# Optimization experiments

Measured on AMD Instinct MI355X. Metric: run time of the kernel, lower is better.

The kernel has to match this reference:

```python
import jax, jax.numpy as jnp
import numpy as np

N_NODES = 100000
N_EDGES = 3200000
BATCH = 16
HIDDEN = 64


def setup_inputs() -> dict:
    key = jax.random.key(0)
    k_mu, k_ei, k_w1, k_b1, k_w2, k_b2 = jax.random.split(key, 6)
    mu = jax.random.normal(k_mu, (BATCH, N_NODES), dtype=jnp.float32)
    edge_index = jax.random.randint(k_ei, (2, N_EDGES), 0, N_NODES, dtype=jnp.int64)
    # MLP params: Linear(1, hidden) -> GELU -> Linear(hidden, 1)
    W1 = jax.random.normal(k_w1, (1, HIDDEN), dtype=jnp.float32) * (1.0 / np.sqrt(1))
    b1 = jax.random.normal(k_b1, (HIDDEN,), dtype=jnp.float32) * 0.02
    W2 = jax.random.normal(k_w2, (HIDDEN, 1), dtype=jnp.float32) * (1.0 / np.sqrt(HIDDEN))
    b2 = jax.random.normal(k_b2, (1,), dtype=jnp.float32) * 0.02
    return {"mu": mu, "edge_index": edge_index, "W1": W1, "b1": b1, "W2": W2, "b2": b2}


def reference(mu, edge_index, W1, b1, W2, b2):
    row, col = edge_index[0], edge_index[1]
    B, N = mu.shape
    # degree of each destination node (clamped at 1)
    deg = jax.ops.segment_sum(jnp.ones_like(row, dtype=mu.dtype), row, num_segments=N)
    deg = jnp.maximum(deg, 1.0)  # [N]
    # batched message aggregation: gather source values, scatter-add to rows
    msgs = mu[:, col].T                                    # [E, B]
    agg = jax.ops.segment_sum(msgs, row, num_segments=N)   # [N, B]
    out = agg.T / deg[None, :]                             # [B, N]
    # tiny MLP applied per scalar: 1 -> hidden -> 1 with exact (erf) GELU
    h = jax.nn.gelu(out[..., None] * W1[0][None, None, :] + b1, approximate=False)  # [B, N, H]
    y = jnp.einsum('bnh,h->bn', h, W2[:, 0]) + b2[0]       # [B, N]
    return y
```

## Files before the change

### kernel.cpp

```cpp
#include <hip/hip_runtime.h>
#include <hip/hip_fp16.h>

#define N_NODES 100000
#define N_EDGES 3200000
#define BATCH   16
#define HIDDEN  64

#define NBINS   512
#define NPB     196
#define CAP_BIN 7168
#define EPB     8192
#define MAXW    14

#define TBLKS   391
#define LBLKS   33

#define LUT_SIZE  8192
#define LUT_LO    (-16.0f)
#define LUT_SCALE (LUT_SIZE / 32.0f)

typedef int v4i __attribute__((ext_vector_type(4)));

__global__ __launch_bounds__(256) void prep_kernel(
    const float* __restrict__ mu, __half* __restrict__ mu_h,
    const float* __restrict__ W1, const float* __restrict__ b1,
    const float* __restrict__ W2, const float* __restrict__ b2,
    float* __restrict__ lut, unsigned int* __restrict__ gcnt) {
  int blk = blockIdx.x;
  int t = threadIdx.x;
  if (blk < TBLKS) {
    int n = blk * 256 + t;
    if (n >= N_NODES) return;
    float4 o[4];
#pragma unroll
    for (int q = 0; q < 4; ++q) {
      o[q].x = mu[(q * 4 + 0) * N_NODES + n];
      o[q].y = mu[(q * 4 + 1) * N_NODES + n];
      o[q].z = mu[(q * 4 + 2) * N_NODES + n];
      o[q].w = mu[(q * 4 + 3) * N_NODES + n];
    }
    __half2 hh[8];
#pragma unroll
    for (int q = 0; q < 4; ++q) {
      hh[2 * q]     = __floats2half2_rn(o[q].x, o[q].y);
      hh[2 * q + 1] = __floats2half2_rn(o[q].z, o[q].w);
    }
    int4 w0 = make_int4(*(int*)&hh[0], *(int*)&hh[1], *(int*)&hh[2], *(int*)&hh[3]);
    int4 w1 = make_int4(*(int*)&hh[4], *(int*)&hh[5], *(int*)&hh[6], *(int*)&hh[7]);
    int4* dst = (int4*)(mu_h + (size_t)n * BATCH);
    dst[0] = w0;
    dst[1] = w1;
  } else if (blk < TBLKS + LBLKS) {
    int i = (blk - TBLKS) * 256 + t;
    if (i > LUT_SIZE) return;
    float x = LUT_LO + (float)i / LUT_SCALE;
    float acc = b2[0];
    for (int h = 0; h < HIDDEN; ++h) {
      float z = fmaf(x, W1[h], b1[h]);
      float g = 0.5f * z * (1.0f + erff(z * 0.70710678118654752f));
      acc = fmaf(g, W2[h], acc);
    }
    lut[i] = acc;
  } else {
    for (int i = t; i < NBINS; i += 256) gcnt[i] = 0u;
  }
}

__global__ __launch_bounds__(512) void partition_kernel(
    const int* __restrict__ ei, unsigned int* __restrict__ gcnt,
    unsigned int* __restrict__ packed) {
  __shared__ int cnt_[NBINS];
  __shared__ int prefix[NBINS];
  __shared__ unsigned int gbase[NBINS];
  __shared__ int wsum[8];
  __shared__ unsigned int stag[EPB];
  __shared__ unsigned short sbin[EPB];

  int t = threadIdx.x;
  int base = blockIdx.x * EPB;
  int nvalid = min(EPB, N_EDGES - base);
  cnt_[t] = 0;
  __syncthreads();

  unsigned int pk[16];
  int bn[16];
  int rk[16];
  if (t * 16 + 16 <= nvalid) {
    const v4i* rp = (const v4i*)(ei + base + t * 16);
    const v4i* cp = (const v4i*)(ei + N_EDGES + base + t * 16);
    v4i rr[4], cc[4];
#pragma unroll
    for (int q = 0; q < 4; ++q) {
      rr[q] = __builtin_nontemporal_load(&rp[q]);
      cc[q] = __builtin_nontemporal_load(&cp[q]);
    }
#pragma unroll
    for (int q = 0; q < 4; ++q) {
#pragma unroll
      for (int u = 0; u < 4; ++u) {
        int k = q * 4 + u;
        int r = rr[q][u];
        int c = cc[q][u];
        int b = r / NPB;
        int rl = r - b * NPB;
        pk[k] = ((unsigned int)rl << 17) | (unsigned int)c;
        bn[k] = b;
      }
    }
#pragma unroll
    for (int k = 0; k < 16; ++k) rk[k] = atomicAdd(&cnt_[bn[k]], 1);
  } else {
#pragma unroll
    for (int k = 0; k < 16; ++k) {
      int e = t * 16 + k;
      if (e < nvalid) {
        int r = ei[base + e];
        int c = ei[N_EDGES + base + e];
        int b = r / NPB;
        int rl = r - b * NPB;
        pk[k] = ((unsigned int)rl << 17) | (unsigned int)c;
        bn[k] = b;
        rk[k] = atomicAdd(&cnt_[b], 1);
      } else {
        bn[k] = -1;
      }
    }
  }
  __syncthreads();

  int lane = t & 63;
  int wid = t >> 6;
  int v = cnt_[t];
  int sv = v;
#pragma unroll
  for (int d = 1; d < 64; d <<= 1) {
    int n = __shfl_up(sv, d, 64);
    if (lane >= d) sv += n;
  }
  if (lane == 63) wsum[wid] = sv;
  __syncthreads();
  if (t < 8) {
    int s = wsum[t];
#pragma unroll
    for (int d = 1; d < 8; d <<= 1) {
      int n = __shfl_up(s, d, 8);
      if (t >= d) s += n;
    }
    wsum[t] = s;
  }
  __syncthreads();
  int incl = sv + (wid ? wsum[wid - 1] : 0);
  prefix[t] = incl - v;

  gbase[t] = v ? atomicAdd(&gcnt[t], (unsigned int)v) : 0u;
  __syncthreads();

#pragma unroll
  for (int k = 0; k < 16; ++k) {
    if (bn[k] >= 0) {
      int p = prefix[bn[k]] + rk[k];
      stag[p] = pk[k];
      sbin[p] = (unsigned short)bn[k];
    }
  }
  __syncthreads();

  for (int i = t; i < nvalid; i += 512) {
    int b = sbin[i];
    unsigned int pos = gbase[b] + (unsigned int)(i - prefix[b]);
    if (pos < CAP_BIN)
      __builtin_nontemporal_store(stag[i], &packed[(size_t)b * CAP_BIN + pos]);
  }
}

__global__ __launch_bounds__(512) void scatter_apply_kernel(
    const unsigned int* __restrict__ gcnt, const unsigned int* __restrict__ packed,
    const __half* __restrict__ mu_h, const float* __restrict__ lut,
    float* __restrict__ out) {
  __shared__ unsigned int scol[CAP_BIN];
  __shared__ int dcnt[NPB];
  __shared__ int ebase[NPB];
  __shared__ int wpart[4];

  int t = threadIdx.x;
  int bin = blockIdx.x;

  int cnt = min((int)gcnt[bin], CAP_BIN);
  const unsigned int* pp = packed + (size_t)bin * CAP_BIN;

  if (t < NPB) dcnt[t] = 0;
  __syncthreads();

  unsigned int w[MAXW];
#pragma unroll
  for (int k = 0; k < MAXW; ++k) w[k] = pp[k * 512 + t];

  int rk[MAXW];
#pragma unroll
  for (int k = 0; k < MAXW; ++k) {
    int i = k * 512 + t;
    rk[k] = (i < cnt) ? atomicAdd(&dcnt[w[k] >> 17], 1) : 0;
  }
  __syncthreads();

  int v = 0, sv = 0;
  if (t < 256) {
    v = (t < NPB) ? dcnt[t] : 0;
    int lane = t & 63;
    sv = v;
#pragma unroll
    for (int d = 1; d < 64; d <<= 1) {
      int n = __shfl_up(sv, d, 64);
      if (lane >= d) sv += n;
    }
    if (lane == 63) wpart[t >> 6] = sv;
  }
  __syncthreads();
  if (t < 256) {
    int wid = t >> 6;
    int off = 0;
#pragma unroll
    for (int q = 0; q < 3; ++q)
      if (wid > q) off += wpart[q];
    if (t < NPB) ebase[t] = sv + off - v;
  }
  __syncthreads();

#pragma unroll
  for (int k = 0; k < MAXW; ++k) {
    int i = k * 512 + t;
    if (i < cnt) {
      int rl = (int)(w[k] >> 17);
      scol[ebase[rl] + rk[k]] = w[k] & 0x1FFFFu;
    }
  }
  __syncthreads();

  const __half2* mu2 = (const __half2*)mu_h;
  int j2 = t & 7;
  int nsl = t >> 3;
  int binBase = bin * NPB;

#pragma unroll
  for (int pass = 0; pass < 4; ++pass) {
    int nl = pass * 64 + nsl;
    if (nl < NPB) {
      int node = binBase + nl;
      if (node < N_NODES) {
        int s = ebase[nl];
        int e = s + dcnt[nl];
        float2 a0 = {0.f, 0.f}, a1 = {0.f, 0.f};
        float2 a2 = {0.f, 0.f}, a3 = {0.f, 0.f};
        int i = s;
        for (; i + 4 <= e; i += 4) {
          int c0 = (int)scol[i];
          int c1 = (int)scol[i + 1];
          int c2 = (int)scol[i + 2];
          int c3 = (int)scol[i + 3];
          __half2 v0 = mu2[(size_t)c0 * 8 + j2];
          __half2 v1 = mu2[(size_t)c1 * 8 + j2];
          __half2 v2 = mu2[(size_t)c2 * 8 + j2];
          __half2 v3 = mu2[(size_t)c3 * 8 + j2];
          float2 f0 = __half22float2(v0);
          float2 f1 = __half22float2(v1);
          float2 f2 = __half22float2(v2);
          float2 f3 = __half22float2(v3);
          a0.x += f0.x; a0.y += f0.y;
          a1.x += f1.x; a1.y += f1.y;
          a2.x += f2.x; a2.y += f2.y;
          a3.x += f3.x; a3.y += f3.y;
        }
        for (; i < e; ++i) {
          float2 f = __half22float2(mu2[(size_t)scol[i] * 8 + j2]);
          a0.x += f.x; a0.y += f.y;
        }
        float sx = (a0.x + a1.x) + (a2.x + a3.x);
        float sy = (a0.y + a1.y) + (a2.y + a3.y);
        float dinv = 1.0f / (float)max(e - s, 1);

        float xs[2] = {sx * dinv, sy * dinv};
#pragma unroll
        for (int q = 0; q < 2; ++q) {
          float u = (xs[q] - LUT_LO) * LUT_SCALE;
          u = fminf(fmaxf(u, 0.0f), (float)LUT_SIZE - 0.001f);
          int ii = (int)u;
          float frac = u - (float)ii;
          float lo = lut[ii];
          float hi = lut[ii + 1];
          __builtin_nontemporal_store(fmaf(hi - lo, frac, lo),
                                      &out[(size_t)(2 * j2 + q) * N_NODES + node]);
        }
      }
    }
  }
}

extern "C" void kernel_launch(void* const* d_in, const int* in_sizes, int n_in,
                              void* d_out, int out_size, void* d_ws, size_t ws_size,
                              hipStream_t stream) {
  const float* mu = (const float*)d_in[0];
  const int*   ei = (const int*)d_in[1];
  const float* W1 = (const float*)d_in[2];
  const float* b1 = (const float*)d_in[3];
  const float* W2 = (const float*)d_in[4];
  const float* b2 = (const float*)d_in[5];
  float* out = (float*)d_out;

  __half* mu_h = (__half*)d_ws;
  float* lut  = (float*)(mu_h + (size_t)N_NODES * BATCH);
  unsigned int* gcnt = (unsigned int*)(lut + LUT_SIZE + 1);
  unsigned int* packed = gcnt + NBINS;

  prep_kernel<<<TBLKS + LBLKS + 1, 256, 0, stream>>>(mu, mu_h, W1, b1, W2, b2, lut, gcnt);

  int pblocks = (N_EDGES + EPB - 1) / EPB;
  partition_kernel<<<pblocks, 512, 0, stream>>>(ei, gcnt, packed);

  scatter_apply_kernel<<<NBINS, 512, 0, stream>>>(gcnt, packed, mu_h, lut, out);
}
```

Measured before the change: 139.2 us.

## Fuse prep and partition kernels into one launch with shared aux array

Merges the mu-to-half transpose and GELU-MLP LUT build into the edge partition kernel as extra block ranges, so the independent work runs concurrently in one launch. The gcnt counter zeroing moves to a hipMemsetAsync. The per-bin global atomic is issued earlier so its latency overlaps the prefix scan. Three shared arrays are collapsed into one reused aux buffer to cut LDS use. The trade-off is one more memset launch and heterogeneous blocks sharing the partition kernel's LDS footprint.

```diff
diff --git a/kernel.cpp b/kernel.cpp
--- a/kernel.cpp
+++ b/kernel.cpp
@@ -12,8 +12,9 @@
 #define EPB     8192
 #define MAXW    14
 
-#define TBLKS   391
-#define LBLKS   33
+#define PBLKS   391
+#define TBLKS   196
+#define LBLKS   17
 
 #define LUT_SIZE  8192
 #define LUT_LO    (-16.0f)
@@ -21,65 +22,62 @@
 
 typedef int v4i __attribute__((ext_vector_type(4)));
 
-__global__ __launch_bounds__(256) void prep_kernel(
+__global__ __launch_bounds__(512) void fused_part_prep_kernel(
+    const int* __restrict__ ei, unsigned int* __restrict__ gcnt,
+    unsigned int* __restrict__ packed,
     const float* __restrict__ mu, __half* __restrict__ mu_h,
     const float* __restrict__ W1, const float* __restrict__ b1,
     const float* __restrict__ W2, const float* __restrict__ b2,
-    float* __restrict__ lut, unsigned int* __restrict__ gcnt) {
-  int blk = blockIdx.x;
-  int t = threadIdx.x;
-  if (blk < TBLKS) {
-    int n = blk * 256 + t;
-    if (n >= N_NODES) return;
-    float4 o[4];
-#pragma unroll
-    for (int q = 0; q < 4; ++q) {
-      o[q].x = mu[(q * 4 + 0) * N_NODES + n];
-      o[q].y = mu[(q * 4 + 1) * N_NODES + n];
-      o[q].z = mu[(q * 4 + 2) * N_NODES + n];
-      o[q].w = mu[(q * 4 + 3) * N_NODES + n];
-    }
-    __half2 hh[8];
-#pragma unroll
-    for (int q = 0; q < 4; ++q) {
-      hh[2 * q]     = __floats2half2_rn(o[q].x, o[q].y);
-      hh[2 * q + 1] = __floats2half2_rn(o[q].z, o[q].w);
-    }
-    int4 w0 = make_int4(*(int*)&hh[0], *(int*)&hh[1], *(int*)&hh[2], *(int*)&hh[3]);
-    int4 w1 = make_int4(*(int*)&hh[4], *(int*)&hh[5], *(int*)&hh[6], *(int*)&hh[7]);
-    int4* dst = (int4*)(mu_h + (size_t)n * BATCH);
-    dst[0] = w0;
-    dst[1] = w1;
-  } else if (blk < TBLKS + LBLKS) {
-    int i = (blk - TBLKS) * 256 + t;
-    if (i > LUT_SIZE) return;
-    float x = LUT_LO + (float)i / LUT_SCALE;
-    float acc = b2[0];
-    for (int h = 0; h < HIDDEN; ++h) {
-      float z = fmaf(x, W1[h], b1[h]);
-      float g = 0.5f * z * (1.0f + erff(z * 0.70710678118654752f));
-      acc = fmaf(g, W2[h], acc);
-    }
-    lut[i] = acc;
-  } else {
-    for (int i = t; i < NBINS; i += 256) gcnt[i] = 0u;
-  }
-}
-
-__global__ __launch_bounds__(512) void partition_kernel(
-    const int* __restrict__ ei, unsigned int* __restrict__ gcnt,
-    unsigned int* __restrict__ packed) {
-  __shared__ int cnt_[NBINS];
-  __shared__ int prefix[NBINS];
-  __shared__ unsigned int gbase[NBINS];
+    float* __restrict__ lut) {
+  __shared__ int aux[NBINS];
   __shared__ int wsum[8];
   __shared__ unsigned int stag[EPB];
   __shared__ unsigned short sbin[EPB];
 
+  int blk = blockIdx.x;
   int t = threadIdx.x;
-  int base = blockIdx.x * EPB;
+
+  if (blk >= PBLKS) {
+    if (blk < PBLKS + TBLKS) {
+      int n = (blk - PBLKS) * 512 + t;
+      if (n >= N_NODES) return;
+      float4 o[4];
+#pragma unroll
+      for (int q = 0; q < 4; ++q) {
+        o[q].x = mu[(q * 4 + 0) * N_NODES + n];
+        o[q].y = mu[(q * 4 + 1) * N_NODES + n];
+        o[q].z = mu[(q * 4 + 2) * N_NODES + n];
+        o[q].w = mu[(q * 4 + 3) * N_NODES + n];
+      }
+      __half2 hh[8];
+#pragma unroll
+      for (int q = 0; q < 4; ++q) {
+        hh[2 * q]     = __floats2half2_rn(o[q].x, o[q].y);
+        hh[2 * q + 1] = __floats2half2_rn(o[q].z, o[q].w);
+      }
+      int4 w0 = make_int4(*(int*)&hh[0], *(int*)&hh[1], *(int*)&hh[2], *(int*)&hh[3]);
+      int4 w1 = make_int4(*(int*)&hh[4], *(int*)&hh[5], *(int*)&hh[6], *(int*)&hh[7]);
+      int4* dst = (int4*)(mu_h + (size_t)n * BATCH);
+      dst[0] = w0;
+      dst[1] = w1;
+    } else {
+      int i = (blk - PBLKS - TBLKS) * 512 + t;
+      if (i > LUT_SIZE) return;
+      float x = LUT_LO + (float)i / LUT_SCALE;
+      float acc = b2[0];
+      for (int h = 0; h < HIDDEN; ++h) {
+        float z = fmaf(x, W1[h], b1[h]);
+        float g = 0.5f * z * (1.0f + erff(z * 0.70710678118654752f));
+        acc = fmaf(g, W2[h], acc);
+      }
+      lut[i] = acc;
+    }
+    return;
+  }
+
+  int base = blk * EPB;
   int nvalid = min(EPB, N_EDGES - base);
-  cnt_[t] = 0;
+  aux[t] = 0;
   __syncthreads();
 
   unsigned int pk[16];
@@ -108,7 +106,7 @@
       }
     }
 #pragma unroll
-    for (int k = 0; k < 16; ++k) rk[k] = atomicAdd(&cnt_[bn[k]], 1);
+    for (int k = 0; k < 16; ++k) rk[k] = atomicAdd(&aux[bn[k]], 1);
   } else {
 #pragma unroll
     for (int k = 0; k < 16; ++k) {
@@ -120,7 +118,7 @@
         int rl = r - b * NPB;
         pk[k] = ((unsigned int)rl << 17) | (unsigned int)c;
         bn[k] = b;
-        rk[k] = atomicAdd(&cnt_[b], 1);
+        rk[k] = atomicAdd(&aux[b], 1);
       } else {
         bn[k] = -1;
       }
@@ -130,7 +128,10 @@
 
   int lane = t & 63;
   int wid = t >> 6;
-  int v = cnt_[t];
+  int v = aux[t];
+
+  unsigned int gb = v ? atomicAdd(&gcnt[t], (unsigned int)v) : 0u;
+
   int sv = v;
 #pragma unroll
   for (int d = 1; d < 64; d <<= 1) {
@@ -149,25 +150,26 @@
     wsum[t] = s;
   }
   __syncthreads();
-  int incl = sv + (wid ? wsum[wid - 1] : 0);
-  prefix[t] = incl - v;
-
-  gbase[t] = v ? atomicAdd(&gcnt[t], (unsigned int)v) : 0u;
+  int pexcl = sv + (wid ? wsum[wid - 1] : 0) - v;
+  aux[t] = pexcl;
   __syncthreads();
 
 #pragma unroll
   for (int k = 0; k < 16; ++k) {
     if (bn[k] >= 0) {
-      int p = prefix[bn[k]] + rk[k];
+      int p = aux[bn[k]] + rk[k];
       stag[p] = pk[k];
       sbin[p] = (unsigned short)bn[k];
     }
   }
   __syncthreads();
 
+  aux[t] = (int)gb - pexcl;
+  __syncthreads();
+
   for (int i = t; i < nvalid; i += 512) {
     int b = sbin[i];
-    unsigned int pos = gbase[b] + (unsigned int)(i - prefix[b]);
+    unsigned int pos = (unsigned int)(i + aux[b]);
     if (pos < CAP_BIN)
       __builtin_nontemporal_store(stag[i], &packed[(size_t)b * CAP_BIN + pos]);
   }
@@ -311,10 +313,10 @@
   unsigned int* gcnt = (unsigned int*)(lut + LUT_SIZE + 1);
   unsigned int* packed = gcnt + NBINS;
 
-  prep_kernel<<<TBLKS + LBLKS + 1, 256, 0, stream>>>(mu, mu_h, W1, b1, W2, b2, lut, gcnt);
-
-  int pblocks = (N_EDGES + EPB - 1) / EPB;
-  partition_kernel<<<pblocks, 512, 0, stream>>>(ei, gcnt, packed);
+  (void)hipMemsetAsync(gcnt, 0, NBINS * sizeof(unsigned int), stream);
+
+  fused_part_prep_kernel<<<PBLKS + TBLKS + LBLKS, 512, 0, stream>>>(
+      ei, gcnt, packed, mu, mu_h, W1, b1, W2, b2, lut);
 
   scatter_apply_kernel<<<NBINS, 512, 0, stream>>>(gcnt, packed, mu_h, lut, out);
 }
```

New measurement: 132.6 us, median of 2. 1.05x faster.
